# Kernel optimization log

Measured on AMD Instinct MI355X. Metric: run time of the kernel, lower is better.

Reference implementation:

```python
import jax, jax.numpy as jnp
import numpy as np

B, T, N_EMBED, HEAD_SIZE = 4096, 50, 600, 100
CHUNK = N_EMBED // HEAD_SIZE  # 6: per-group input channels of the grouped 1x1 conv


def _grouped_proj(x, w):
    # Conv1d(kernel=1, groups=HEAD_SIZE, bias=False): output channel h is a dot
    # product of its weight row with the h-th CHUNK-slice of the embedding.
    xr = x.reshape(x.shape[0], x.shape[1], HEAD_SIZE, CHUNK)  # [B,T,H,chunk]
    return jnp.einsum('bthc,hc->bth', xr, w)  # [B,T,HEAD_SIZE]


def setup_inputs() -> dict:
    key = jax.random.key(0)
    k0, k1, k2, k3 = jax.random.split(key, 4)
    scale = 1.0 / np.sqrt(CHUNK)
    x = jax.random.normal(k0, (B, T, N_EMBED), dtype=jnp.float32)
    w_q = jax.random.normal(k1, (HEAD_SIZE, CHUNK), dtype=jnp.float32) * scale
    w_k = jax.random.normal(k2, (HEAD_SIZE, CHUNK), dtype=jnp.float32) * scale
    w_v = jax.random.normal(k3, (HEAD_SIZE, CHUNK), dtype=jnp.float32) * scale
    return {"x": x, "w_q": w_q, "w_k": w_k, "w_v": w_v}


def reference(x, w_q, w_k, w_v):
    Bx, Tx, C = x.shape
    q = _grouped_proj(x, w_q)  # [B,T,H]
    k = _grouped_proj(x, w_k)  # [B,T,H]
    v = _grouped_proj(x, w_v)  # [B,T,H]
    # scores scaled by full embed dim C (as in the source), causal mask, softmax
    wei = jnp.einsum('bth,bsh->bts', q, k) * (C ** -0.5)  # [B,T,T]
    causal = jnp.tril(jnp.ones((Tx, Tx), dtype=bool))
    wei = jnp.where(causal, wei, -jnp.inf)
    wei = jax.nn.softmax(wei, axis=-1)
    out = jnp.einsum('bts,bsh->bth', wei, v)  # [B,T,HEAD_SIZE]
    return out
```

## Files before the change

kernel.cpp:

```cpp
#include <hip/hip_runtime.h>


#define BATCH 4096
#define TT 50
#define HH 100
#define CC 600

typedef __attribute__((ext_vector_type(8))) short short8;
typedef __attribute__((ext_vector_type(4))) short short4v;
typedef __attribute__((ext_vector_type(4))) float f32x4;
typedef unsigned short ushort_t;

constexpr int NTHR = 256;
constexpr int NWAVES = NTHR / 64;
constexpr float kScale = 0.04082482904638630163f;

constexpr int OQ = 0, OKk = 6400, OV = 12800, OP = 19968, LDS_US = 24064;

__device__ __forceinline__ ushort_t f2bf(float f) {
    unsigned u = __float_as_uint(f);
    u += 0x7FFFu + ((u >> 16) & 1u);
    return (ushort_t)(u >> 16);
}
__device__ __forceinline__ float bf2f(ushort_t h) {
    return __uint_as_float(((unsigned)h) << 16);
}

__global__ __launch_bounds__(NTHR, 3) void headc_fused(
    const float* __restrict__ x,
    const float* __restrict__ wq,
    const float* __restrict__ wk,
    const float* __restrict__ wv,
    float* __restrict__ out)
{
    __shared__ __align__(16) ushort_t lds[LDS_US];

    const int b = blockIdx.x;
    const int tid = threadIdx.x;
    const float* xb = x + (size_t)b * (TT * CC);

    for (int i = tid; i < 2496; i += NTHR) {
        short8 z = {0, 0, 0, 0, 0, 0, 0, 0};
        *reinterpret_cast<short8*>(lds + i * 8) = z;
    }
    __syncthreads();

    for (int j = tid; j < 650; j += NTHR) {
        const int qd = j / 50;
        const int hp = j - qd * 50;
        const int h0 = hp * 2;
        const int tbase = qd * 4;

        float4 xr[4][3];
        #pragma unroll
        for (int r = 0; r < 4; ++r) {
            const int tc = (tbase + r < TT) ? (tbase + r) : (TT - 1);
            const float* xp = xb + tc * CC + h0 * 6;
            xr[r][0] = *(const float4*)xp;
            xr[r][1] = *(const float4*)(xp + 4);
            xr[r][2] = *(const float4*)(xp + 8);
        }
        const float4 wqa = *(const float4*)(wq + h0 * 6);
        const float4 wqb = *(const float4*)(wq + h0 * 6 + 4);
        const float4 wqc = *(const float4*)(wq + h0 * 6 + 8);
        const float4 wka = *(const float4*)(wk + h0 * 6);
        const float4 wkb = *(const float4*)(wk + h0 * 6 + 4);
        const float4 wkc = *(const float4*)(wk + h0 * 6 + 8);
        const float4 wva = *(const float4*)(wv + h0 * 6);
        const float4 wvb = *(const float4*)(wv + h0 * 6 + 4);
        const float4 wvc = *(const float4*)(wv + h0 * 6 + 8);

        short4v vp0 = {0, 0, 0, 0};
        short4v vp1 = {0, 0, 0, 0};
        #pragma unroll
        for (int r = 0; r < 4; ++r) {
            const int t = tbase + r;
            const float4 xa = xr[r][0], xm = xr[r][1], xc = xr[r][2];
            float q0 = xa.x*wqa.x + xa.y*wqa.y + xa.z*wqa.z + xa.w*wqa.w + xm.x*wqb.x + xm.y*wqb.y;
            float q1 = xm.z*wqb.z + xm.w*wqb.w + xc.x*wqc.x + xc.y*wqc.y + xc.z*wqc.z + xc.w*wqc.w;
            float k0 = xa.x*wka.x + xa.y*wka.y + xa.z*wka.z + xa.w*wka.w + xm.x*wkb.x + xm.y*wkb.y;
            float k1 = xm.z*wkb.z + xm.w*wkb.w + xc.x*wkc.x + xc.y*wkc.y + xc.z*wkc.z + xc.w*wkc.w;
            float v0 = xa.x*wva.x + xa.y*wva.y + xa.z*wva.z + xa.w*wva.w + xm.x*wvb.x + xm.y*wvb.y;
            float v1 = xm.z*wvb.z + xm.w*wvb.w + xc.x*wvc.x + xc.y*wvc.y + xc.z*wvc.z + xc.w*wvc.w;
            q0 *= kScale; q1 *= kScale;
            if (t < TT) {
                const int qg = (((h0 >> 3) ^ (t & 7)) << 3) + (h0 & 7);
                *reinterpret_cast<unsigned*>(lds + OQ  + t * 128 + qg) =
                    (unsigned)f2bf(q0) | ((unsigned)f2bf(q1) << 16);
                *reinterpret_cast<unsigned*>(lds + OKk + t * 128 + qg) =
                    (unsigned)f2bf(k0) | ((unsigned)f2bf(k1) << 16);
                vp0[r] = (short)f2bf(v0);
                vp1[r] = (short)f2bf(v1);
            }
        }
        const int g = qd >> 1, half = (qd & 1) * 4;
        *reinterpret_cast<short4v*>(lds + OV + h0 * 64 + ((g ^ (h0 & 7)) << 3) + half) = vp0;
        *reinterpret_cast<short4v*>(lds + OV + (h0 + 1) * 64 + ((g ^ ((h0 + 1) & 7)) << 3) + half) = vp1;
    }
    __syncthreads();

    const int wv_ = tid >> 6;
    const int lane = tid & 63;
    const int l15 = lane & 15, l4 = lane >> 4;

    for (int p = wv_; p < 10; p += NWAVES) {
        const int tm = (p >= 6) ? 3 : (p >= 3) ? 2 : (p >= 1) ? 1 : 0;
        const int sn = p - tm * (tm + 1) / 2;
        f32x4 acc = {0.f, 0.f, 0.f, 0.f};
        const int ar = tm * 16 + l15;
        const int br = sn * 16 + l15;
        #pragma unroll
        for (int kk = 0; kk < 4; ++kk) {
            const int g = kk * 4 + l4;
            const short8 a  = *reinterpret_cast<const short8*>(lds + OQ  + ar * 128 + ((g ^ (ar & 7)) << 3));
            const short8 bb = *reinterpret_cast<const short8*>(lds + OKk + br * 128 + ((g ^ (br & 7)) << 3));
            acc = __builtin_amdgcn_mfma_f32_16x16x32_bf16(a, bb, acc, 0, 0, 0);
        }
        const int row0 = tm * 16 + l4 * 4;
        const int col = sn * 16 + l15;
        #pragma unroll
        for (int r = 0; r < 4; ++r) {
            const int row = row0 + r;
            lds[OP + row * 64 + (((col >> 3) ^ (row & 7)) << 3) + (col & 7)] = f2bf(acc[r]);
        }
    }
    __syncthreads();

    if (tid < TT) {
        const int t = tid;
        float vv[64];
        float mx = -3.4e38f;
        #pragma unroll
        for (int g = 0; g < 8; ++g) {
            const short8 pk = *reinterpret_cast<const short8*>(lds + OP + t * 64 + ((g ^ (t & 7)) << 3));
            #pragma unroll
            for (int jj = 0; jj < 8; ++jj) {
                const int s = g * 8 + jj;
                const float f = bf2f((ushort_t)pk[jj]);
                vv[s] = f;
                mx = (s <= t) ? fmaxf(mx, f) : mx;
            }
        }
        float sum = 0.f;
        #pragma unroll
        for (int s = 0; s < 64; ++s) {
            const float e = (s <= t) ? __expf(vv[s] - mx) : 0.f;
            vv[s] = e;
            sum += e;
        }
        const float inv = 1.f / sum;
        #pragma unroll
        for (int g = 0; g < 8; ++g) {
            short8 w;
            #pragma unroll
            for (int jj = 0; jj < 8; ++jj) w[jj] = (short)f2bf(vv[g * 8 + jj] * inv);
            *reinterpret_cast<short8*>(lds + OP + t * 64 + ((g ^ (t & 7)) << 3)) = w;
        }
    }
    __syncthreads();

    float* ob = out + (size_t)b * (TT * HH);
    for (int p = wv_; p < 28; p += NWAVES) {
        const int tm = p / 7, hn = p - tm * 7;
        f32x4 acc = {0.f, 0.f, 0.f, 0.f};
        const int ar = tm * 16 + l15;
        const int br = hn * 16 + l15;
        #pragma unroll
        for (int kk = 0; kk < 2; ++kk) {
            const int g = kk * 4 + l4;
            const short8 a  = *reinterpret_cast<const short8*>(lds + OP + ar * 64 + ((g ^ (ar & 7)) << 3));
            const short8 bb = *reinterpret_cast<const short8*>(lds + OV + br * 64 + ((g ^ (br & 7)) << 3));
            acc = __builtin_amdgcn_mfma_f32_16x16x32_bf16(a, bb, acc, 0, 0, 0);
        }
        const int h = hn * 16 + l15;
        const int t0 = tm * 16 + l4 * 4;
        if (h < HH) {
            #pragma unroll
            for (int r = 0; r < 4; ++r) {
                const int t = t0 + r;
                if (t < TT) ob[t * HH + h] = acc[r];
            }
        }
    }
}

extern "C" void kernel_launch(void* const* d_in, const int* in_sizes, int n_in,
                              void* d_out, int out_size, void* d_ws, size_t ws_size,
                              hipStream_t stream) {
    const float* x  = (const float*)d_in[0];
    const float* wq = (const float*)d_in[1];
    const float* wk = (const float*)d_in[2];
    const float* wv = (const float*)d_in[3];
    float* out = (float*)d_out;
    headc_fused<<<dim3(BATCH), dim3(NTHR), 0, stream>>>(x, wq, wk, wv, out);
}
```

Measured before the change: 132.8 us.

## Parallelize softmax across four lanes per row and trim LDS zero-fill

Softmax now runs with four threads per query row, combining partial max and sum through shuffles, where before a single thread handled each row. The full LDS zero-fill and its barrier are replaced by targeted zeroing of only the padding regions, done in parallel with the projection phase. The projection loop is reshaped so each thread loads the weights once and handles up to three time quads. The bf16 conversion also switches to the library intrinsic. The change risks correctness if any padding region the MMA reads is left unzeroed, and shuffle correctness depends on the four lanes of a row sitting in the same wave.

```diff
diff --git a/kernel.cpp b/kernel.cpp
--- a/kernel.cpp
+++ b/kernel.cpp
@@ -1,4 +1,5 @@
 #include <hip/hip_runtime.h>
+#include <hip/hip_bf16.h>
 
 
 #define BATCH 4096
@@ -12,15 +13,13 @@
 typedef unsigned short ushort_t;
 
 constexpr int NTHR = 256;
-constexpr int NWAVES = NTHR / 64;
+constexpr int NWAVES = 4;
 constexpr float kScale = 0.04082482904638630163f;
 
 constexpr int OQ = 0, OKk = 6400, OV = 12800, OP = 19968, LDS_US = 24064;
 
 __device__ __forceinline__ ushort_t f2bf(float f) {
-    unsigned u = __float_as_uint(f);
-    u += 0x7FFFu + ((u >> 16) & 1u);
-    return (ushort_t)(u >> 16);
+    return __builtin_bit_cast(ushort_t, __float2bfloat16(f));
 }
 __device__ __forceinline__ float bf2f(ushort_t h) {
     return __uint_as_float(((unsigned)h) << 16);
@@ -39,27 +38,41 @@
     const int tid = threadIdx.x;
     const float* xb = x + (size_t)b * (TT * CC);
 
-    for (int i = tid; i < 2496; i += NTHR) {
-        short8 z = {0, 0, 0, 0, 0, 0, 0, 0};
-        *reinterpret_cast<short8*>(lds + i * 8) = z;
-    }
-    __syncthreads();
-
-    for (int j = tid; j < 650; j += NTHR) {
-        const int qd = j / 50;
-        const int hp = j - qd * 50;
+    {
+        const short8 z8 = {0, 0, 0, 0, 0, 0, 0, 0};
+        const short4v z4 = {0, 0, 0, 0};
+        if (tid < 100) {
+            const int arr = tid / 50;
+            const int r = tid % 50;
+            const int base = (arr ? OKk : OQ) + r * 128;
+            *reinterpret_cast<short4v*>(lds + base + ((12 ^ (r & 7)) << 3) + 4) = z4;
+            *reinterpret_cast<short8*>(lds + base + ((13 ^ (r & 7)) << 3)) = z8;
+            *reinterpret_cast<short8*>(lds + base + ((14 ^ (r & 7)) << 3)) = z8;
+            *reinterpret_cast<short8*>(lds + base + ((15 ^ (r & 7)) << 3)) = z8;
+            #pragma unroll
+            for (int rr = 0; rr < 2; ++rr) {
+                const int vr = tid + rr * 100;
+                if (vr < 100) {
+                    *reinterpret_cast<short4v*>(lds + OV + vr * 64 + ((6 ^ (vr & 7)) << 3) + 4) = z4;
+                    *reinterpret_cast<short8*>(lds + OV + vr * 64 + ((7 ^ (vr & 7)) << 3)) = z8;
+                }
+            }
+        } else if (tid < 196) {
+            const int idx = tid - 100;
+            const int r = 100 + (idx >> 3);
+            const int gr = idx & 7;
+            *reinterpret_cast<short8*>(lds + OV + r * 64 + gr * 8) = z8;
+        } else if (tid < 246) {
+            const int vr = tid - 196 + 50;
+            *reinterpret_cast<short4v*>(lds + OV + vr * 64 + ((6 ^ (vr & 7)) << 3) + 4) = z4;
+            *reinterpret_cast<short8*>(lds + OV + vr * 64 + ((7 ^ (vr & 7)) << 3)) = z8;
+        }
+    }
+
+    if (tid < 250) {
+        const int hp = tid % 50;
+        const int c  = tid / 50;
         const int h0 = hp * 2;
-        const int tbase = qd * 4;
-
-        float4 xr[4][3];
-        #pragma unroll
-        for (int r = 0; r < 4; ++r) {
-            const int tc = (tbase + r < TT) ? (tbase + r) : (TT - 1);
-            const float* xp = xb + tc * CC + h0 * 6;
-            xr[r][0] = *(const float4*)xp;
-            xr[r][1] = *(const float4*)(xp + 4);
-            xr[r][2] = *(const float4*)(xp + 8);
-        }
         const float4 wqa = *(const float4*)(wq + h0 * 6);
         const float4 wqb = *(const float4*)(wq + h0 * 6 + 4);
         const float4 wqc = *(const float4*)(wq + h0 * 6 + 8);
@@ -70,32 +83,48 @@
         const float4 wvb = *(const float4*)(wv + h0 * 6 + 4);
         const float4 wvc = *(const float4*)(wv + h0 * 6 + 8);
 
-        short4v vp0 = {0, 0, 0, 0};
-        short4v vp1 = {0, 0, 0, 0};
-        #pragma unroll
-        for (int r = 0; r < 4; ++r) {
-            const int t = tbase + r;
-            const float4 xa = xr[r][0], xm = xr[r][1], xc = xr[r][2];
-            float q0 = xa.x*wqa.x + xa.y*wqa.y + xa.z*wqa.z + xa.w*wqa.w + xm.x*wqb.x + xm.y*wqb.y;
-            float q1 = xm.z*wqb.z + xm.w*wqb.w + xc.x*wqc.x + xc.y*wqc.y + xc.z*wqc.z + xc.w*wqc.w;
-            float k0 = xa.x*wka.x + xa.y*wka.y + xa.z*wka.z + xa.w*wka.w + xm.x*wkb.x + xm.y*wkb.y;
-            float k1 = xm.z*wkb.z + xm.w*wkb.w + xc.x*wkc.x + xc.y*wkc.y + xc.z*wkc.z + xc.w*wkc.w;
-            float v0 = xa.x*wva.x + xa.y*wva.y + xa.z*wva.z + xa.w*wva.w + xm.x*wvb.x + xm.y*wvb.y;
-            float v1 = xm.z*wvb.z + xm.w*wvb.w + xc.x*wvc.x + xc.y*wvc.y + xc.z*wvc.z + xc.w*wvc.w;
-            q0 *= kScale; q1 *= kScale;
-            if (t < TT) {
-                const int qg = (((h0 >> 3) ^ (t & 7)) << 3) + (h0 & 7);
-                *reinterpret_cast<unsigned*>(lds + OQ  + t * 128 + qg) =
-                    (unsigned)f2bf(q0) | ((unsigned)f2bf(q1) << 16);
-                *reinterpret_cast<unsigned*>(lds + OKk + t * 128 + qg) =
-                    (unsigned)f2bf(k0) | ((unsigned)f2bf(k1) << 16);
-                vp0[r] = (short)f2bf(v0);
-                vp1[r] = (short)f2bf(v1);
-            }
-        }
-        const int g = qd >> 1, half = (qd & 1) * 4;
-        *reinterpret_cast<short4v*>(lds + OV + h0 * 64 + ((g ^ (h0 & 7)) << 3) + half) = vp0;
-        *reinterpret_cast<short4v*>(lds + OV + (h0 + 1) * 64 + ((g ^ ((h0 + 1) & 7)) << 3) + half) = vp1;
+        #pragma unroll
+        for (int u = 0; u < 3; ++u) {
+            const int qd = c + u * 5;
+            if (qd <= 12) {
+                const int tbase = qd * 4;
+                float4 xr[4][3];
+                #pragma unroll
+                for (int r = 0; r < 4; ++r) {
+                    const int tc = (tbase + r < TT) ? (tbase + r) : (TT - 1);
+                    const float* xp = xb + tc * CC + h0 * 6;
+                    xr[r][0] = *(const float4*)xp;
+                    xr[r][1] = *(const float4*)(xp + 4);
+                    xr[r][2] = *(const float4*)(xp + 8);
+                }
+                short4v vp0 = {0, 0, 0, 0};
+                short4v vp1 = {0, 0, 0, 0};
+                #pragma unroll
+                for (int r = 0; r < 4; ++r) {
+                    const int t = tbase + r;
+                    const float4 xa = xr[r][0], xm = xr[r][1], xc = xr[r][2];
+                    float q0 = xa.x*wqa.x + xa.y*wqa.y + xa.z*wqa.z + xa.w*wqa.w + xm.x*wqb.x + xm.y*wqb.y;
+                    float q1 = xm.z*wqb.z + xm.w*wqb.w + xc.x*wqc.x + xc.y*wqc.y + xc.z*wqc.z + xc.w*wqc.w;
+                    float k0 = xa.x*wka.x + xa.y*wka.y + xa.z*wka.z + xa.w*wka.w + xm.x*wkb.x + xm.y*wkb.y;
+                    float k1 = xm.z*wkb.z + xm.w*wkb.w + xc.x*wkc.x + xc.y*wkc.y + xc.z*wkc.z + xc.w*wkc.w;
+                    float v0 = xa.x*wva.x + xa.y*wva.y + xa.z*wva.z + xa.w*wva.w + xm.x*wvb.x + xm.y*wvb.y;
+                    float v1 = xm.z*wvb.z + xm.w*wvb.w + xc.x*wvc.x + xc.y*wvc.y + xc.z*wvc.z + xc.w*wvc.w;
+                    q0 *= kScale; q1 *= kScale;
+                    if (t < TT) {
+                        const int qg = (((h0 >> 3) ^ (t & 7)) << 3) + (h0 & 7);
+                        *reinterpret_cast<unsigned*>(lds + OQ  + t * 128 + qg) =
+                            (unsigned)f2bf(q0) | ((unsigned)f2bf(q1) << 16);
+                        *reinterpret_cast<unsigned*>(lds + OKk + t * 128 + qg) =
+                            (unsigned)f2bf(k0) | ((unsigned)f2bf(k1) << 16);
+                        vp0[r] = (short)f2bf(v0);
+                        vp1[r] = (short)f2bf(v1);
+                    }
+                }
+                const int g = qd >> 1, half = (qd & 1) * 4;
+                *reinterpret_cast<short4v*>(lds + OV + h0 * 64 + ((g ^ (h0 & 7)) << 3) + half) = vp0;
+                *reinterpret_cast<short4v*>(lds + OV + (h0 + 1) * 64 + ((g ^ ((h0 + 1) & 7)) << 3) + half) = vp1;
+            }
+        }
     }
     __syncthreads();
 
@@ -126,35 +155,47 @@
     }
     __syncthreads();
 
-    if (tid < TT) {
-        const int t = tid;
-        float vv[64];
-        float mx = -3.4e38f;
-        #pragma unroll
-        for (int g = 0; g < 8; ++g) {
-            const short8 pk = *reinterpret_cast<const short8*>(lds + OP + t * 64 + ((g ^ (t & 7)) << 3));
-            #pragma unroll
-            for (int jj = 0; jj < 8; ++jj) {
-                const int s = g * 8 + jj;
-                const float f = bf2f((ushort_t)pk[jj]);
-                vv[s] = f;
-                mx = (s <= t) ? fmaxf(mx, f) : mx;
-            }
-        }
-        float sum = 0.f;
-        #pragma unroll
-        for (int s = 0; s < 64; ++s) {
-            const float e = (s <= t) ? __expf(vv[s] - mx) : 0.f;
-            vv[s] = e;
-            sum += e;
-        }
-        const float inv = 1.f / sum;
-        #pragma unroll
-        for (int g = 0; g < 8; ++g) {
-            short8 w;
-            #pragma unroll
-            for (int jj = 0; jj < 8; ++jj) w[jj] = (short)f2bf(vv[g * 8 + jj] * inv);
-            *reinterpret_cast<short8*>(lds + OP + t * 64 + ((g ^ (t & 7)) << 3)) = w;
+    {
+        const int t = tid >> 2, ll = tid & 3;
+        if (t < TT) {
+            const int ga = (2 * ll) ^ (t & 7), gb = (2 * ll + 1) ^ (t & 7);
+            const short8 pa = *reinterpret_cast<const short8*>(lds + OP + t * 64 + (ga << 3));
+            const short8 pb = *reinterpret_cast<const short8*>(lds + OP + t * 64 + (gb << 3));
+            float v[16];
+            float mx = -3.4e38f;
+            #pragma unroll
+            for (int j = 0; j < 8; ++j) {
+                const int s = 16 * ll + j;
+                v[j] = bf2f((ushort_t)pa[j]);
+                if (s <= t) mx = fmaxf(mx, v[j]);
+            }
+            #pragma unroll
+            for (int j = 0; j < 8; ++j) {
+                const int s = 16 * ll + 8 + j;
+                v[8 + j] = bf2f((ushort_t)pb[j]);
+                if (s <= t) mx = fmaxf(mx, v[8 + j]);
+            }
+            mx = fmaxf(mx, __shfl_xor(mx, 1));
+            mx = fmaxf(mx, __shfl_xor(mx, 2));
+            float sum = 0.f;
+            #pragma unroll
+            for (int j = 0; j < 16; ++j) {
+                const int s = 16 * ll + j;
+                const float e = (s <= t) ? __expf(v[j] - mx) : 0.f;
+                v[j] = e;
+                sum += e;
+            }
+            sum += __shfl_xor(sum, 1);
+            sum += __shfl_xor(sum, 2);
+            const float inv = 1.f / sum;
+            short8 wa, wb;
+            #pragma unroll
+            for (int j = 0; j < 8; ++j) {
+                wa[j] = (short)f2bf(v[j] * inv);
+                wb[j] = (short)f2bf(v[8 + j] * inv);
+            }
+            *reinterpret_cast<short8*>(lds + OP + t * 64 + (ga << 3)) = wa;
+            *reinterpret_cast<short8*>(lds + OP + t * 64 + (gb << 3)) = wb;
         }
     }
     __syncthreads();
```

Result: faster. 121.5 us (-8.5%).
